# Performance work log

Hardware: AMD Instinct MI355X
Metric: run time of the kernel (lower is better)

The kernel has to match this reference:

```python
import jax, jax.numpy as jnp
import numpy as np

DIM = 1024
HEADS = 16
DIM_HEAD = DIM // HEADS
SCALE = DIM_HEAD ** -0.5
LN_EPS = 1e-5


def setup_inputs() -> dict:
    key = jax.random.key(0)
    ks = jax.random.split(key, 7)
    b, n = 4, 2048
    x = jax.random.normal(ks[0], (b, n, DIM), dtype=jnp.float32)
    pos = jax.random.normal(ks[1], (b, n, DIM), dtype=jnp.float32)
    # params (torch Linear init-like scale)
    w_qkv = jax.random.normal(ks[2], (DIM, 3 * DIM), dtype=jnp.float32) * (DIM ** -0.5)
    w_out = jax.random.normal(ks[3], (DIM, DIM), dtype=jnp.float32) * (DIM ** -0.5)
    b_out = jax.random.normal(ks[4], (DIM,), dtype=jnp.float32) * 0.01
    ln_gamma = jnp.ones((DIM,), dtype=jnp.float32)
    ln_beta = jnp.zeros((DIM,), dtype=jnp.float32)
    return {"x": x, "pos": pos, "w_qkv": w_qkv, "w_out": w_out,
            "b_out": b_out, "ln_gamma": ln_gamma, "ln_beta": ln_beta}


def _layer_norm(x, gamma, beta):
    mu = jnp.mean(x, axis=-1, keepdims=True)
    var = jnp.mean(jnp.square(x - mu), axis=-1, keepdims=True)
    return (x - mu) * jax.lax.rsqrt(var + LN_EPS) * gamma + beta


def reference(x, pos, w_qkv, w_out, b_out, ln_gamma, ln_beta):
    b, n, _ = x.shape
    xn = _layer_norm(x, ln_gamma, ln_beta)
    qkv = xn @ w_qkv                                    # [b, n, 3*dim]
    q, k, v = jnp.split(qkv, 3, axis=-1)
    # [b, n, dim] -> [b, h, n, d]
    to_heads = lambda t: t.reshape(b, n, HEADS, DIM_HEAD).transpose(0, 2, 1, 3)
    q, k, v = to_heads(q), to_heads(k), to_heads(v)
    scores = jnp.einsum('bhid,bhjd->bhij', q, k) * SCALE  # [b, h, n, n]
    attn = jax.nn.softmax(scores, axis=-1)
    out = jnp.einsum('bhij,bhjd->bhid', attn, v)          # [b, h, n, d]
    out = out.transpose(0, 2, 1, 3).reshape(b, n, DIM)    # [b, n, dim]
    return (out + pos) @ w_out + b_out
```

## Files before the change

kernel.cpp:

```cpp
#include <hip/hip_runtime.h>
#include <math.h>
#include <stdint.h>

#define TOKENS 8192
#define DIM 1024
#define N3 3072
#define NSEQ 2048
#define NH 16
#define DH 64

typedef __attribute__((ext_vector_type(8))) __bf16 bf16x8;
typedef __attribute__((ext_vector_type(4))) float f32x4;
typedef __attribute__((ext_vector_type(16))) float f32x16;
typedef __attribute__((ext_vector_type(4))) short short4v;

__device__ __forceinline__ unsigned cvt2bf(float a, float b) {
    unsigned r;
    asm("v_cvt_pk_bf16_f32 %0, %1, %2" : "=v"(r) : "v"(a), "v"(b));
    return r;
}
__device__ __forceinline__ unsigned short f2bf(float f) {
    unsigned r;
    asm("v_cvt_pk_bf16_f32 %0, %1, %1" : "=v"(r) : "v"(f));
    return (unsigned short)r;
}
__device__ __forceinline__ float exp2_raw(float x) {
    float r;
    asm("v_exp_f32 %0, %1" : "=v"(r) : "v"(x));
    return r;
}

__device__ __forceinline__ void glds16(const void* g, void* l) {
    __builtin_amdgcn_global_load_lds((__attribute__((address_space(1))) void*)(void*)g,
                                     (__attribute__((address_space(3))) void*)l, 16, 0, 0);
}

__global__ __launch_bounds__(256) void transpose_to_bf16(
    const float* __restrict__ in, unsigned short* __restrict__ out, int R, int C) {
    __shared__ float tile[64][65];
    int n0 = blockIdx.x * 64, k0 = blockIdx.y * 64;
    int t = threadIdx.x;
#pragma unroll
    for (int i = 0; i < 16; i++) {
        int idx = i * 256 + t;
        int r = idx >> 6, c = idx & 63;
        tile[r][c] = in[(size_t)(k0 + r) * C + n0 + c];
    }
    __syncthreads();
#pragma unroll
    for (int i = 0; i < 16; i++) {
        int idx = i * 256 + t;
        int r = idx >> 6, c = idx & 63;
        out[(size_t)(n0 + r) * R + k0 + c] = f2bf(tile[c][r]);
    }
}

__global__ __launch_bounds__(256) void ln_kernel(
    const float* __restrict__ x, const float* __restrict__ gamma,
    const float* __restrict__ beta, unsigned short* __restrict__ xn) {
    int row = blockIdx.x;
    int t = threadIdx.x;
    const float4 v = ((const float4*)(x + (size_t)row * DIM))[t];
    float s = v.x + v.y + v.z + v.w;
    float sq = v.x * v.x + v.y * v.y + v.z * v.z + v.w * v.w;
#pragma unroll
    for (int m = 1; m < 64; m <<= 1) {
        s += __shfl_xor(s, m);
        sq += __shfl_xor(sq, m);
    }
    __shared__ float ws[4], wq[4];
    int w = t >> 6, lane = t & 63;
    if (lane == 0) { ws[w] = s; wq[w] = sq; }
    __syncthreads();
    s = ws[0] + ws[1] + ws[2] + ws[3];
    sq = wq[0] + wq[1] + wq[2] + wq[3];
    float mu = s * (1.0f / DIM);
    float var = sq * (1.0f / DIM) - mu * mu;
    float rstd = rsqrtf(var + 1e-5f);
    const float4 g = ((const float4*)gamma)[t];
    const float4 bb = ((const float4*)beta)[t];
    uint2 o;
    o.x = cvt2bf((v.x - mu) * rstd * g.x + bb.x, (v.y - mu) * rstd * g.y + bb.y);
    o.y = cvt2bf((v.z - mu) * rstd * g.z + bb.z, (v.w - mu) * rstd * g.w + bb.w);
    *(uint2*)(xn + (size_t)row * DIM + t * 4) = o;
}

__device__ __forceinline__ void xcd_swizzle(int& bx, int& by) {
    int nwgx = gridDim.x;
    int nwg = nwgx * gridDim.y;
    int wg = by * nwgx + bx;
    int cpx = nwg >> 3;
    int swz = (wg & 7) * cpx + (wg >> 3);
    bx = swz % nwgx;
    by = swz / nwgx;
}

__device__ __forceinline__ void gemm_core8(
    const unsigned short* __restrict__ A, const unsigned short* __restrict__ Bt, int K,
    int brow, int bcol, char* As, char* Bs, f32x4 acc[2][4]) {
    int t = threadIdx.x, w = t >> 6, lane = t & 63;
    int wm = w >> 1, wn = w & 1;
    int srow = lane >> 2, scol = (lane & 3) * 8;
    const char* sA = (const char*)(A + (size_t)(brow + w * 16 + srow) * K + scol);
    const char* sB = (const char*)(Bt + (size_t)(bcol + w * 16 + srow) * K + scol);
    char* a0 = As; char* a1 = As + 8192; char* a2 = As + 16384;
    char* b0 = Bs; char* b1 = Bs + 8192; char* b2 = Bs + 16384;
    auto stage = [&](int k0, char* ab, char* bb) {
        glds16(sA + (size_t)k0 * 2, ab + w * 1024);
        glds16(sB + (size_t)k0 * 2, bb + w * 1024);
    };
    stage(0, a0, b0);
    stage(32, a1, b1);
    int NT = K >> 5;
    for (int kt = 0; kt < NT; kt++) {
        asm volatile("s_waitcnt vmcnt(2)" ::: "memory");
        __builtin_amdgcn_s_barrier();
        int kn = kt + 2; if (kn >= NT) kn -= NT;
        stage(kn << 5, a2, b2);
        bf16x8 a[2], b[4];
#pragma unroll
        for (int i = 0; i < 2; i++)
            a[i] = *(const bf16x8*)(a0 + (wm * 32 + i * 16 + (lane & 15)) * 64 + (lane >> 4) * 16);
#pragma unroll
        for (int j = 0; j < 4; j++)
            b[j] = *(const bf16x8*)(b0 + (wn * 64 + j * 16 + (lane & 15)) * 64 + (lane >> 4) * 16);
        __builtin_amdgcn_s_setprio(1);
#pragma unroll
        for (int i = 0; i < 2; i++)
#pragma unroll
            for (int j = 0; j < 4; j++)
                acc[i][j] = __builtin_amdgcn_mfma_f32_16x16x32_bf16(a[i], b[j], acc[i][j], 0, 0, 0);
        __builtin_amdgcn_s_setprio(0);
        char* tp;
        tp = a0; a0 = a1; a1 = a2; a2 = tp;
        tp = b0; b0 = b1; b1 = b2; b2 = tp;
    }
}

#define QSCALE_LOG2E 0.18033688011112042f

__global__ __launch_bounds__(512, 6) void gemm_qkv(
    const unsigned short* __restrict__ A, const unsigned short* __restrict__ Bt,
    unsigned short* __restrict__ Qb, unsigned short* __restrict__ Kb,
    unsigned short* __restrict__ Vt) {
    __shared__ __align__(16) char As[3 * 8192];
    __shared__ __align__(16) char Bs[3 * 8192];
    int bx = blockIdx.x, by = blockIdx.y;
    xcd_swizzle(bx, by);
    int brow = by * 128, bcol = bx * 128;
    f32x4 acc[2][4] = {};
    gemm_core8(A, Bt, DIM, brow, bcol, As, Bs, acc);

    int t = threadIdx.x, w = t >> 6, lane = t & 63;
    int wm = w >> 1, wn = w & 1;
    int part = bcol >> 10;
#pragma unroll
    for (int i = 0; i < 2; i++) {
#pragma unroll
        for (int j = 0; j < 4; j++) {
            int col = bcol + wn * 64 + j * 16 + (lane & 15);
            int within = col & 1023;
            int h = within >> 6, d = within & 63;
            int rowb = brow + wm * 32 + i * 16 + (lane >> 4) * 4;
            if (part == 2) {
                int b = rowb >> 11, n = rowb & 2047;
                int bh = (b << 4) + h;
                uint2 pv;
                pv.x = cvt2bf(acc[i][j][0], acc[i][j][1]);
                pv.y = cvt2bf(acc[i][j][2], acc[i][j][3]);
                *(uint2*)(Vt + ((size_t)bh * 64 + d) * 2048 + n) = pv;
            } else {
#pragma unroll
                for (int r = 0; r < 4; r++) {
                    int row = rowb + r;
                    int b = row >> 11, n = row & 2047;
                    int bh = (b << 4) + h;
                    float val = acc[i][j][r];
                    if (part == 0)
                        Qb[((size_t)bh * 2048 + n) * 64 + d] = f2bf(val * QSCALE_LOG2E);
                    else
                        Kb[((size_t)bh * 2048 + n) * 64 + d] = f2bf(val);
                }
            }
        }
    }
}

__global__ __launch_bounds__(512, 6) void gemm_out(
    const unsigned short* __restrict__ A, const unsigned short* __restrict__ Bt,
    const float* __restrict__ bias, float* __restrict__ out) {
    __shared__ __align__(16) char As[3 * 8192];
    __shared__ __align__(16) char Bs[3 * 8192];
    int bx = blockIdx.x, by = blockIdx.y;
    xcd_swizzle(bx, by);
    int brow = by * 128, bcol = bx * 128;
    f32x4 acc[2][4] = {};
    gemm_core8(A, Bt, DIM, brow, bcol, As, Bs, acc);

    int t = threadIdx.x, w = t >> 6, lane = t & 63;
    int wm = w >> 1, wn = w & 1;
#pragma unroll
    for (int i = 0; i < 2; i++) {
#pragma unroll
        for (int j = 0; j < 4; j++) {
            int col = bcol + wn * 64 + j * 16 + (lane & 15);
            float bv = bias[col];
#pragma unroll
            for (int r = 0; r < 4; r++) {
                int row = brow + wm * 32 + i * 16 + (lane >> 4) * 4 + r;
                out[(size_t)row * DIM + col] = acc[i][j][r] + bv;
            }
        }
    }
}

__global__ __launch_bounds__(512, 4) void attn_kernel(
    const unsigned short* __restrict__ Qb, const unsigned short* __restrict__ Kb,
    const unsigned short* __restrict__ Vt, const float* __restrict__ pos,
    unsigned short* __restrict__ att) {
    __shared__ __align__(16) char Ks[4][8192];
    __shared__ __align__(16) char Vs[4][8192];
    int t = threadIdx.x, w = t >> 6, lane = t & 63;
    int l31 = lane & 31, lhi = lane >> 5;

    int L = blockIdx.y * gridDim.x + blockIdx.x;
    int bh = (L & 7) + (((L >> 3) & 7) << 3);
    int qt = L >> 6;
    int b = bh >> 4, h = bh & 15;
    int qr = qt * 256 + w * 32 + l31;

    const unsigned short* Qh = Qb + (size_t)bh * NSEQ * DH;
    const char* Khc = (const char*)(Kb + (size_t)bh * NSEQ * DH);
    const char* Vhc = (const char*)(Vt + (size_t)bh * DH * NSEQ);

    bf16x8 qf[4];
#pragma unroll
    for (int ks = 0; ks < 4; ks++)
        qf[ks] = *(const bf16x8*)(Qh + (size_t)qr * DH + ks * 16 + lhi * 8);

    f32x16 oacc[2] = {};
    float lsum = 0.f;

    int ct = w >> 2, cs = w & 3;
    const char* Ksrc = Khc + (size_t)(ct * 32 + l31) * 128 + cs * 32 + lhi * 16;
    const char* Vsrc = Vhc + (size_t)(ct * 32 + l31) * 4096 + (size_t)(cs * 16 + lhi * 8) * 2;
    auto stage = [&](char* kbuf, char* vbuf, int kv0) {
        glds16(Ksrc + (size_t)kv0 * 128, kbuf + w * 1024);
        glds16(Vsrc + (size_t)kv0 * 2, vbuf + w * 1024);
    };

    auto compute = [&](const char* kc, const char* vc) {
        f32x16 st0 = {}, st1 = {};
        __builtin_amdgcn_s_setprio(1);
#pragma unroll
        for (int ks = 0; ks < 4; ks++) {
            bf16x8 kf = *(const bf16x8*)(kc + ks * 1024 + lane * 16);
            st0 = __builtin_amdgcn_mfma_f32_32x32x16_bf16(kf, qf[ks], st0, 0, 0, 0);
        }
#pragma unroll
        for (int ks = 0; ks < 4; ks++) {
            bf16x8 kf = *(const bf16x8*)(kc + (4 + ks) * 1024 + lane * 16);
            st1 = __builtin_amdgcn_mfma_f32_32x32x16_bf16(kf, qf[ks], st1, 0, 0, 0);
        }
        __builtin_amdgcn_s_setprio(0);

        {
            float s0 = 0.f, s1 = 0.f, s2 = 0.f, s3 = 0.f;
#pragma unroll
            for (int r = 0; r < 16; r += 4) {
                float e0 = exp2_raw(st0[r]);
                float e1 = exp2_raw(st0[r + 1]);
                float e2 = exp2_raw(st0[r + 2]);
                float e3 = exp2_raw(st0[r + 3]);
                st0[r] = e0; st0[r + 1] = e1; st0[r + 2] = e2; st0[r + 3] = e3;
                s0 += e0; s1 += e1; s2 += e2; s3 += e3;
            }
#pragma unroll
            for (int r = 0; r < 16; r += 4) {
                float e0 = exp2_raw(st1[r]);
                float e1 = exp2_raw(st1[r + 1]);
                float e2 = exp2_raw(st1[r + 2]);
                float e3 = exp2_raw(st1[r + 3]);
                st1[r] = e0; st1[r + 1] = e1; st1[r + 2] = e2; st1[r + 3] = e3;
                s0 += e0; s1 += e1; s2 += e2; s3 += e3;
            }
            lsum += (s0 + s1) + (s2 + s3);
        }
        bf16x8 bfr[4];
#pragma unroll
        for (int ks = 0; ks < 4; ks++) {
            const f32x16& sv = (ks < 2) ? st0 : st1;
            int rb = (ks & 1) * 8;
            unsigned pa = cvt2bf(sv[rb + 0], sv[rb + 1]);
            unsigned pc = cvt2bf(sv[rb + 2], sv[rb + 3]);
            unsigned pb = cvt2bf(sv[rb + 4], sv[rb + 5]);
            unsigned pd = cvt2bf(sv[rb + 6], sv[rb + 7]);
            asm("v_permlane32_swap_b32 %0, %1" : "+v"(pa), "+v"(pb));
            asm("v_permlane32_swap_b32 %0, %1" : "+v"(pc), "+v"(pd));
            uint4 pw = {pa, pc, pb, pd};
            bfr[ks] = *(bf16x8*)&pw;
        }
        __builtin_amdgcn_s_setprio(1);
#pragma unroll
        for (int ks = 0; ks < 4; ks++)
#pragma unroll
            for (int dt = 0; dt < 2; dt++) {
                bf16x8 vf = *(const bf16x8*)(vc + (dt * 4 + ks) * 1024 + lane * 16);
                oacc[dt] = __builtin_amdgcn_mfma_f32_32x32x16_bf16(vf, bfr[ks], oacc[dt], 0, 0, 0);
            }
        __builtin_amdgcn_s_setprio(0);
    };

    char* kA0 = Ks[0]; char* kA1 = Ks[1]; char* kB0 = Ks[2]; char* kB1 = Ks[3];
    char* vA0 = Vs[0]; char* vA1 = Vs[1]; char* vB0 = Vs[2]; char* vB1 = Vs[3];
    stage(kA0, vA0, 0);
    stage(kA1, vA1, 64);

    for (int p = 0; p < 32; p += 2) {
        asm volatile("s_waitcnt vmcnt(2)" ::: "memory");
        __builtin_amdgcn_s_barrier();
        stage(kB0, vB0, ((p + 2) & 31) << 6);
        stage(kB1, vB1, ((p + 3) & 31) << 6);
        compute(kA0, vA0);
        asm volatile("s_waitcnt vmcnt(4)" ::: "memory");
        compute(kA1, vA1);
        char* tp;
        tp = kA0; kA0 = kB0; kB0 = tp;  tp = kA1; kA1 = kB1; kB1 = tp;
        tp = vA0; vA0 = vB0; vB0 = tp;  tp = vA1; vA1 = vB1; vB1 = tp;
    }

    {
        float pa = lsum, pb = lsum;
        asm("v_permlane32_swap_b32 %0, %1" : "+v"(pa), "+v"(pb));
        lsum = pa + pb;
    }
    float inv = 1.0f / lsum;
    size_t rowbase = ((size_t)b * NSEQ + qr) * DIM + h * 64;
#pragma unroll
    for (int dt = 0; dt < 2; dt++)
#pragma unroll
        for (int g4 = 0; g4 < 4; g4++) {
            int d = dt * 32 + g4 * 8 + lhi * 4;
            float4 pv = *(const float4*)(pos + rowbase + d);
            uint2 o;
            o.x = cvt2bf(oacc[dt][g4 * 4 + 0] * inv + pv.x, oacc[dt][g4 * 4 + 1] * inv + pv.y);
            o.y = cvt2bf(oacc[dt][g4 * 4 + 2] * inv + pv.z, oacc[dt][g4 * 4 + 3] * inv + pv.w);
            *(uint2*)(att + rowbase + d) = o;
        }
}

extern "C" void kernel_launch(void* const* d_in, const int* in_sizes, int n_in,
                              void* d_out, int out_size, void* d_ws, size_t ws_size,
                              hipStream_t stream) {
    const float* x = (const float*)d_in[0];
    const float* pos = (const float*)d_in[1];
    const float* w_qkv = (const float*)d_in[2];
    const float* w_out = (const float*)d_in[3];
    const float* b_out = (const float*)d_in[4];
    const float* ln_g = (const float*)d_in[5];
    const float* ln_b = (const float*)d_in[6];
    float* out = (float*)d_out;

    char* ws = (char*)d_ws;
    unsigned short* xn      = (unsigned short*)(ws);
    unsigned short* wqkv_bt = (unsigned short*)(ws + (16ull << 20));
    unsigned short* wout_bt = (unsigned short*)(ws + (22ull << 20));
    unsigned short* Qb      = (unsigned short*)(ws + (24ull << 20));
    unsigned short* Kb      = (unsigned short*)(ws + (40ull << 20));
    unsigned short* Vt      = (unsigned short*)(ws + (56ull << 20));
    unsigned short* att     = xn;

    transpose_to_bf16<<<dim3(N3 / 64, DIM / 64), 256, 0, stream>>>(w_qkv, wqkv_bt, DIM, N3);
    transpose_to_bf16<<<dim3(DIM / 64, DIM / 64), 256, 0, stream>>>(w_out, wout_bt, DIM, DIM);
    ln_kernel<<<TOKENS, 256, 0, stream>>>(x, ln_g, ln_b, xn);
    gemm_qkv<<<dim3(N3 / 128, TOKENS / 128), 512, 0, stream>>>(xn, wqkv_bt, Qb, Kb, Vt);
    attn_kernel<<<dim3(NSEQ / 256, 64), 512, 0, stream>>>(Qb, Kb, Vt, pos, att);
    gemm_out<<<dim3(DIM / 128, TOKENS / 128), 512, 0, stream>>>(att, wout_bt, b_out, out);
}
```

Baseline: 194.7 us.

## Software-pipeline QK of next tile with softmax/PV of current in attention

Restructures the attention main loop to work on 32-key tiles in a 4-slot shared ring buffer that holds K and V together. Waves 0-3 load K and waves 4-7 load V. The QK^T MFMAs for the next tile are issued before the exp/convert/PV work of the current tile, so the matrix and vector units can overlap. Shared memory use is halved, from 64KB to 32KB, which may allow more resident blocks. In exchange there are twice as many barriers per key, and the ring-buffer wait counts and the prologue, plus redundant wrap-around loads at the tail, must stay correct.

```diff
diff --git a/kernel.cpp b/kernel.cpp
--- a/kernel.cpp
+++ b/kernel.cpp
@@ -218,8 +218,7 @@
     const unsigned short* __restrict__ Qb, const unsigned short* __restrict__ Kb,
     const unsigned short* __restrict__ Vt, const float* __restrict__ pos,
     unsigned short* __restrict__ att) {
-    __shared__ __align__(16) char Ks[4][8192];
-    __shared__ __align__(16) char Vs[4][8192];
+    __shared__ __align__(16) char KV[4][8192];
     int t = threadIdx.x, w = t >> 6, lane = t & 63;
     int l31 = lane & 31, lhi = lane >> 5;
 
@@ -241,56 +240,46 @@
     f32x16 oacc[2] = {};
     float lsum = 0.f;
 
-    int ct = w >> 2, cs = w & 3;
-    const char* Ksrc = Khc + (size_t)(ct * 32 + l31) * 128 + cs * 32 + lhi * 16;
-    const char* Vsrc = Vhc + (size_t)(ct * 32 + l31) * 4096 + (size_t)(cs * 16 + lhi * 8) * 2;
-    auto stage = [&](char* kbuf, char* vbuf, int kv0) {
-        glds16(Ksrc + (size_t)kv0 * 128, kbuf + w * 1024);
-        glds16(Vsrc + (size_t)kv0 * 2, vbuf + w * 1024);
+    const char* srcBase;
+    size_t strideT;
+    if (w < 4) {
+        srcBase = Khc + (size_t)l31 * 128 + w * 32 + lhi * 16;
+        strideT = 32 * 128;
+    } else {
+        int c = w - 4, dt = c >> 1, ks = c & 1;
+        srcBase = Vhc + (size_t)(dt * 32 + l31) * 4096 + (size_t)(ks * 16 + lhi * 8) * 2;
+        strideT = 32 * 2;
+    }
+    auto stage = [&](char* buf, int tl) {
+        glds16(srcBase + (size_t)tl * strideT, buf + w * 1024);
     };
 
-    auto compute = [&](const char* kc, const char* vc) {
-        f32x16 st0 = {}, st1 = {};
-        __builtin_amdgcn_s_setprio(1);
+    auto QK = [&](const char* kc) -> f32x16 {
+        f32x16 s = {};
 #pragma unroll
         for (int ks = 0; ks < 4; ks++) {
             bf16x8 kf = *(const bf16x8*)(kc + ks * 1024 + lane * 16);
-            st0 = __builtin_amdgcn_mfma_f32_32x32x16_bf16(kf, qf[ks], st0, 0, 0, 0);
-        }
-#pragma unroll
-        for (int ks = 0; ks < 4; ks++) {
-            bf16x8 kf = *(const bf16x8*)(kc + (4 + ks) * 1024 + lane * 16);
-            st1 = __builtin_amdgcn_mfma_f32_32x32x16_bf16(kf, qf[ks], st1, 0, 0, 0);
-        }
-        __builtin_amdgcn_s_setprio(0);
-
-        {
-            float s0 = 0.f, s1 = 0.f, s2 = 0.f, s3 = 0.f;
-#pragma unroll
-            for (int r = 0; r < 16; r += 4) {
-                float e0 = exp2_raw(st0[r]);
-                float e1 = exp2_raw(st0[r + 1]);
-                float e2 = exp2_raw(st0[r + 2]);
-                float e3 = exp2_raw(st0[r + 3]);
-                st0[r] = e0; st0[r + 1] = e1; st0[r + 2] = e2; st0[r + 3] = e3;
-                s0 += e0; s1 += e1; s2 += e2; s3 += e3;
-            }
-#pragma unroll
-            for (int r = 0; r < 16; r += 4) {
-                float e0 = exp2_raw(st1[r]);
-                float e1 = exp2_raw(st1[r + 1]);
-                float e2 = exp2_raw(st1[r + 2]);
-                float e3 = exp2_raw(st1[r + 3]);
-                st1[r] = e0; st1[r + 1] = e1; st1[r + 2] = e2; st1[r + 3] = e3;
-                s0 += e0; s1 += e1; s2 += e2; s3 += e3;
-            }
-            lsum += (s0 + s1) + (s2 + s3);
-        }
-        bf16x8 bfr[4];
-#pragma unroll
-        for (int ks = 0; ks < 4; ks++) {
-            const f32x16& sv = (ks < 2) ? st0 : st1;
-            int rb = (ks & 1) * 8;
+            s = __builtin_amdgcn_mfma_f32_32x32x16_bf16(kf, qf[ks], s, 0, 0, 0);
+        }
+        return s;
+    };
+
+    auto FIN = [&](f32x16& sv, const char* vc) {
+        float s0 = 0.f, s1 = 0.f, s2 = 0.f, s3 = 0.f;
+#pragma unroll
+        for (int r = 0; r < 16; r += 4) {
+            float e0 = exp2_raw(sv[r]);
+            float e1 = exp2_raw(sv[r + 1]);
+            float e2 = exp2_raw(sv[r + 2]);
+            float e3 = exp2_raw(sv[r + 3]);
+            sv[r] = e0; sv[r + 1] = e1; sv[r + 2] = e2; sv[r + 3] = e3;
+            s0 += e0; s1 += e1; s2 += e2; s3 += e3;
+        }
+        lsum += (s0 + s1) + (s2 + s3);
+        bf16x8 bfr[2];
+#pragma unroll
+        for (int ks = 0; ks < 2; ks++) {
+            int rb = ks * 8;
             unsigned pa = cvt2bf(sv[rb + 0], sv[rb + 1]);
             unsigned pc = cvt2bf(sv[rb + 2], sv[rb + 3]);
             unsigned pb = cvt2bf(sv[rb + 4], sv[rb + 5]);
@@ -302,31 +291,35 @@
         }
         __builtin_amdgcn_s_setprio(1);
 #pragma unroll
-        for (int ks = 0; ks < 4; ks++)
+        for (int ks = 0; ks < 2; ks++)
 #pragma unroll
             for (int dt = 0; dt < 2; dt++) {
-                bf16x8 vf = *(const bf16x8*)(vc + (dt * 4 + ks) * 1024 + lane * 16);
+                bf16x8 vf = *(const bf16x8*)(vc + 4096 + (dt * 2 + ks) * 1024 + lane * 16);
                 oacc[dt] = __builtin_amdgcn_mfma_f32_32x32x16_bf16(vf, bfr[ks], oacc[dt], 0, 0, 0);
             }
         __builtin_amdgcn_s_setprio(0);
     };
 
-    char* kA0 = Ks[0]; char* kA1 = Ks[1]; char* kB0 = Ks[2]; char* kB1 = Ks[3];
-    char* vA0 = Vs[0]; char* vA1 = Vs[1]; char* vB0 = Vs[2]; char* vB1 = Vs[3];
-    stage(kA0, vA0, 0);
-    stage(kA1, vA1, 64);
-
-    for (int p = 0; p < 32; p += 2) {
-        asm volatile("s_waitcnt vmcnt(2)" ::: "memory");
+    char* q0 = KV[0]; char* q1 = KV[1]; char* q2 = KV[2]; char* q3 = KV[3];
+    stage(q0, 0); stage(q1, 1); stage(q2, 2);
+    asm volatile("s_waitcnt vmcnt(2)" ::: "memory");
+    __builtin_amdgcn_s_barrier();
+    f32x16 sP = QK(q0);
+    f32x16 sN;
+
+    for (int tl = 0; tl < 64; tl += 2) {
+        asm volatile("s_waitcnt vmcnt(1)" ::: "memory");
         __builtin_amdgcn_s_barrier();
-        stage(kB0, vB0, ((p + 2) & 31) << 6);
-        stage(kB1, vB1, ((p + 3) & 31) << 6);
-        compute(kA0, vA0);
-        asm volatile("s_waitcnt vmcnt(4)" ::: "memory");
-        compute(kA1, vA1);
-        char* tp;
-        tp = kA0; kA0 = kB0; kB0 = tp;  tp = kA1; kA1 = kB1; kB1 = tp;
-        tp = vA0; vA0 = vB0; vB0 = tp;  tp = vA1; vA1 = vB1; vB1 = tp;
+        stage(q3, (tl + 3) & 63);
+        sN = QK(q1);
+        FIN(sP, q0);
+        asm volatile("s_waitcnt vmcnt(1)" ::: "memory");
+        __builtin_amdgcn_s_barrier();
+        stage(q0, (tl + 4) & 63);
+        sP = QK(q2);
+        FIN(sN, q1);
+        char* tp0 = q0; char* tp1 = q1;
+        q0 = q2; q1 = q3; q2 = tp0; q3 = tp1;
     }
 
     {
```

Result: no change. 194.7 us (+0.0%).
